# Performance work log

Measured on AMD Instinct MI355X. Metric: run time of the kernel, lower is better.

Reference implementation:

```python
import jax, jax.numpy as jnp
import numpy as np

BITS = 4
N_PACK = 32 // BITS  # int32 compression
GROUPSIZE = 128
MASK = (1 << BITS) - 1


def _unpack_int32(q, axis):
    """Unpack int32 tensor into N_PACK low-bit values along `axis`.
    Element j*N_PACK+e comes from bits [BITS*e, BITS*(e+1)) of packed word j."""
    parts = [ (q >> (BITS * e)) & MASK for e in range(N_PACK) ]
    u = jnp.stack(parts, axis=axis + 1)  # (..., P, N_PACK, ...)
    shape = list(q.shape)
    shape[axis] = shape[axis] * N_PACK
    return u.reshape(shape)


def setup_inputs() -> dict:
    key = jax.random.key(0)
    k1, k2, k3, k4, k5 = jax.random.split(key, 5)
    in_f, out_f = 4096, 12288
    tokens = 8192
    n_groups = in_f // GROUPSIZE  # 32
    x = jax.random.normal(k1, (tokens, in_f), dtype=jnp.float32)
    scales = jax.random.uniform(k2, (n_groups, out_f), dtype=jnp.float32) * 0.01 + 1e-3
    bias = jax.random.normal(k3, (out_f,), dtype=jnp.float32)
    qweight = jax.random.randint(k4, (in_f // N_PACK, out_f), jnp.iinfo(jnp.int32).min, jnp.iinfo(jnp.int32).max, dtype=jnp.int32)
    qzeros = jax.random.randint(k5, (n_groups, out_f // N_PACK), jnp.iinfo(jnp.int32).min, jnp.iinfo(jnp.int32).max, dtype=jnp.int32)
    return {"x": x, "scales": scales, "bias": bias, "qweight": qweight, "qzeros": qzeros}


def reference(x, scales, bias, qweight, qzeros):
    in_f = qweight.shape[0] * N_PACK
    out_f = qweight.shape[1]
    n_groups = scales.shape[0]
    # Unpack 4-bit weights along input-channel axis: (in_f, out_f), values 0..15
    w_int = _unpack_int32(qweight, axis=0).astype(scales.dtype)
    # Unpack zero points along output-channel axis; optimum format stores zp-1
    zp = (_unpack_int32(qzeros, axis=1) + 1).astype(scales.dtype)  # (n_groups, out_f)
    # Per-group dequant: group g covers input channels [g*GROUPSIZE, (g+1)*GROUPSIZE)
    w = (w_int.reshape(n_groups, GROUPSIZE, out_f) - zp[:, None, :]) * scales[:, None, :]
    w = w.reshape(in_f, out_f)
    # Linear: y = x @ W^T with W = w.T, i.e. x @ w
    return x @ w + bias
```

## Files before the change

kernel.cpp:

```cpp
#include <hip/hip_runtime.h>
#include <hip/hip_bf16.h>


typedef __attribute__((ext_vector_type(8))) short short8;
typedef __attribute__((ext_vector_type(4))) float f32x4;

__device__ __forceinline__ short f2bf(float f) {
  unsigned u = __float_as_uint(f);
  u += 0x7fffu + ((u >> 16) & 1u);
  return (short)(u >> 16);
}

__device__ __forceinline__ void gload_lds16(const void* g, void* l) {
  __builtin_amdgcn_global_load_lds(
      (const __attribute__((address_space(1))) void*)g,
      (__attribute__((address_space(3))) void*)l,
      16, 0, 0);
}

__device__ __forceinline__ void bar() {
  asm volatile("" ::: "memory");
  __builtin_amdgcn_s_barrier();
  asm volatile("" ::: "memory");
}
__device__ __forceinline__ void wait_vm3() {
  asm volatile("s_waitcnt vmcnt(3)" ::: "memory");
}
__device__ __forceinline__ void wait_vm0() {
  asm volatile("s_waitcnt vmcnt(0)" ::: "memory");
}

__global__ __launch_bounds__(256) void dequant_tile_kernel(
    const int* __restrict__ qweight, const int* __restrict__ qzeros,
    const float* __restrict__ scales, short* __restrict__ Bt,
    int N, int K) {
  const int ktn = K >> 5;
  const int bx = blockIdx.x;
  const int nb = bx / ktn, kt = bx - nb * ktn;
  const int t = threadIdx.x;
  const int g = kt >> 2;
  char* dst = (char*)Bt + (size_t)bx * 8192;
#pragma unroll
  for (int p = 0; p < 2; ++p) {
    const int c = p * 256 + t;
    const int l = c & 63;
    const int n = nb * 128 + (c >> 6) * 16 + (l & 15);
    const int kw = kt * 4 + (l >> 4);
    const float sc = scales[(size_t)g * N + n];
    const int zw = qzeros[(size_t)g * (N >> 3) + (n >> 3)];
    const float zs = -(float)(((zw >> ((n & 7) * 4)) & 15) + 1) * sc;
    const int w = qweight[(size_t)kw * N + n];
    short8 v;
#pragma unroll
    for (int e = 0; e < 8; ++e)
      v[e] = f2bf(fmaf((float)((w >> (4 * e)) & 15), sc, zs));
    *(short8*)(dst + c * 16) = v;
  }
}

__global__ __launch_bounds__(256) void cvt_tile_kernel(
    const float* __restrict__ x, short* __restrict__ xb, int K) {
  const int ktn = K >> 5;
  const int bx = blockIdx.x;
  const int mb = bx / ktn, kt = bx - mb * ktn;
  char* dst = (char*)xb + (size_t)bx * 16384;
#pragma unroll
  for (int p = 0; p < 4; ++p) {
    const int c = p * 256 + threadIdx.x;
    const int l = c & 63;
    const int row = mb * 256 + (c >> 6) * 16 + (l & 15);
    const int k = kt * 32 + (l >> 4) * 8;
    const float* s = x + (size_t)row * K + k;
    float4 f0 = *(const float4*)s;
    float4 f1 = *(const float4*)(s + 4);
    short8 v;
    v[0] = f2bf(f0.x); v[1] = f2bf(f0.y); v[2] = f2bf(f0.z); v[3] = f2bf(f0.w);
    v[4] = f2bf(f1.x); v[5] = f2bf(f1.y); v[6] = f2bf(f1.z); v[7] = f2bf(f1.w);
    *(short8*)(dst + c * 16) = v;
  }
}

#define GBM 256
#define GBN 128

__global__ __launch_bounds__(512, 4) void gemm256_kernel(
    const short* __restrict__ At, const short* __restrict__ Bt,
    const float* __restrict__ bias, float* __restrict__ C,
    int M, int N, int K) {
  __shared__ __align__(16) char lds[3 * 24576];
  const int tid = threadIdx.x;
  const int nbx = N / GBN;
  const int nwg = gridDim.x;
  int bid = blockIdx.x;
  if ((nwg & 7) == 0) bid = (bid & 7) * (nwg >> 3) + (bid >> 3);
  const int mb = bid / nbx;
  const int nb = bid % nbx;
  const int bm = mb * GBM, bn = nb * GBN;

  const int wid = tid >> 6, lane = tid & 63;
  const int wr = wid >> 2, wc = wid & 3;

  const int P = K >> 5;

  char* lb = &lds[0];

  const char* aBase = lb + wr * 8192 + lane * 16;
  const char* bBase = lb + 16384 + wc * 2048 + lane * 16;

  const char* pA = (const char*)At + (size_t)mb * P * 16384 + (size_t)tid * 16;
  const char* pB = (const char*)Bt + (size_t)nb * P * 8192 + (size_t)tid * 16;
  char* dA = lb + tid * 16;
  char* dB = lb + 16384 + tid * 16;

#define STAGE(TSL, AOFF, BOFF)                         \
  do {                                                 \
    gload_lds16(pA + (AOFF), dA + (TSL)*24576);        \
    gload_lds16(pA + (AOFF) + 8192, dA + (TSL)*24576 + 8192); \
    gload_lds16(pB + (BOFF), dB + (TSL)*24576);        \
  } while (0)

  short8 aR[8], bR[2];

#define RD(SL)                                                        \
  do {                                                                \
    _Pragma("unroll") for (int i = 0; i < 8; ++i) aR[i] =             \
        *(const short8*)(aBase + (SL)*24576 + i * 1024);              \
    _Pragma("unroll") for (int j = 0; j < 2; ++j) bR[j] =             \
        *(const short8*)(bBase + (SL)*24576 + j * 1024);              \
  } while (0)

  f32x4 acc[8][2] = {};

#define MFMA16()                                                      \
  do {                                                                \
    __builtin_amdgcn_s_setprio(1);                                    \
    _Pragma("unroll") for (int i = 0; i < 8; ++i)                     \
        _Pragma("unroll") for (int j = 0; j < 2; ++j) acc[i][j] =     \
            __builtin_amdgcn_mfma_f32_16x16x32_bf16(aR[i], bR[j],     \
                                                    acc[i][j], 0, 0, 0); \
    __builtin_amdgcn_s_setprio(0);                                    \
  } while (0)

  STAGE(0, 0, 0);
  STAGE(1, 16384, 8192);

  const int nIt = (P - 2) / 3;
  for (int it = 0; it < nIt; ++it) {
    wait_vm3(); bar();
    RD(0); STAGE(2, 2 * 16384, 2 * 8192); MFMA16();
    wait_vm3(); bar();
    RD(1); STAGE(0, 3 * 16384, 3 * 8192); MFMA16();
    wait_vm3(); bar();
    RD(2); STAGE(1, 4 * 16384, 4 * 8192); MFMA16();
    pA += 3 * 16384;
    pB += 3 * 8192;
  }
  wait_vm3(); bar();
  RD(0); MFMA16();
  wait_vm0(); bar();
  RD(1); MFMA16();

#undef MFMA16
#undef RD
#undef STAGE

  const int crow0 = bm + wr * 128 + (lane >> 4) * 4;
  const int ccol0 = bn + wc * 32 + (lane & 15);
#pragma unroll
  for (int fj = 0; fj < 2; ++fj) {
    const float bv = bias[ccol0 + fj * 16];
#pragma unroll
    for (int fi = 0; fi < 8; ++fi) {
#pragma unroll
      for (int r = 0; r < 4; ++r) {
        C[(size_t)(crow0 + fi * 16 + r) * N + ccol0 + fj * 16] =
            acc[fi][fj][r] + bv;
      }
    }
  }
}

__global__ __launch_bounds__(256) void dequant_kernel(
    const int* __restrict__ qweight, const int* __restrict__ qzeros,
    const float* __restrict__ scales, short* __restrict__ Wt,
    int in_f, int out_f) {
  __shared__ __align__(16) short T[64][72];
  const int n0 = blockIdx.x * 64;
  const int k0 = blockIdx.y * 64;
  const int t = threadIdx.x;
  const int nl = t & 63;
  const int kw = t >> 6;
  const int n = n0 + nl;
  const int g = k0 >> 7;
  const float sc = scales[(size_t)g * out_f + n];
  const int zpw = qzeros[(size_t)g * (out_f >> 3) + (n >> 3)];
  const float zp = (float)(((zpw >> ((n & 7) * 4)) & 15) + 1);
  const float zs = zp * sc;
#pragma unroll
  for (int rr = 0; rr < 2; ++rr) {
    const int kwi = kw + rr * 4;
    const int w = qweight[(size_t)((k0 >> 3) + kwi) * out_f + n];
    short8 v;
#pragma unroll
    for (int e = 0; e < 8; ++e) {
      float f = (float)((w >> (4 * e)) & 15) * sc - zs;
      v[e] = f2bf(f);
    }
    *(short8*)&T[nl][kwi * 8] = v;
  }
  __syncthreads();
#pragma unroll
  for (int rr = 0; rr < 2; ++rr) {
    const int c = rr * 256 + t;
    const int row = c >> 3, ch = c & 7;
    *(short8*)&Wt[(size_t)(n0 + row) * in_f + k0 + ch * 8] =
        *(const short8*)&T[row][ch * 8];
  }
}

__global__ __launch_bounds__(256) void cvt_kernel(
    const float* __restrict__ x, short* __restrict__ xb, long n8) {
  long i = (long)blockIdx.x * blockDim.x + threadIdx.x;
  if (i >= n8) return;
  const float* src = x + i * 8;
  float4 a = *(const float4*)src;
  float4 b = *(const float4*)(src + 4);
  short8 v;
  v[0] = f2bf(a.x); v[1] = f2bf(a.y); v[2] = f2bf(a.z); v[3] = f2bf(a.w);
  v[4] = f2bf(b.x); v[5] = f2bf(b.y); v[6] = f2bf(b.z); v[7] = f2bf(b.w);
  *(short8*)(xb + i * 8) = v;
}

#define BM 128
#define BN 128
#define BK 64

template <bool A_BF16>
__global__ __launch_bounds__(256) void gemm_bias_kernel(
    const void* __restrict__ Av, const short* __restrict__ Bt,
    const float* __restrict__ bias, float* __restrict__ C,
    int M, int N, int K) {
  __shared__ __align__(16) short As[BM * BK];
  __shared__ __align__(16) short Bs[BN * BK];
  const int tid = threadIdx.x;
  const int bm = blockIdx.y * BM;
  const int bn = blockIdx.x * BN;
  const int wid = tid >> 6, lane = tid & 63;
  const int wr = wid >> 1, wc = wid & 1;
  const int lrow = lane & 15;
  const int lk = (lane >> 4) * 8;

  f32x4 acc[4][4] = {};

  for (int kt = 0; kt < K; kt += BK) {
    if constexpr (A_BF16) {
      const short* A = (const short*)Av;
#pragma unroll
      for (int r = 0; r < 4; ++r) {
        const int c = r * 256 + tid;
        const int row = c >> 3, ch = c & 7;
        gload_lds16(A + (size_t)(bm + row) * K + kt + ch * 8,
                    (char*)As + c * 16);
      }
    } else {
      const float* A = (const float*)Av;
#pragma unroll
      for (int r = 0; r < 4; ++r) {
        const int c = r * 256 + tid;
        const int row = c >> 3, ch = c & 7;
        const float* src = A + (size_t)(bm + row) * K + kt + ch * 8;
        float4 f0 = *(const float4*)src;
        float4 f1 = *(const float4*)(src + 4);
        short8 v;
        v[0] = f2bf(f0.x); v[1] = f2bf(f0.y); v[2] = f2bf(f0.z); v[3] = f2bf(f0.w);
        v[4] = f2bf(f1.x); v[5] = f2bf(f1.y); v[6] = f2bf(f1.z); v[7] = f2bf(f1.w);
        *(short8*)((char*)As + c * 16) = v;
      }
    }
#pragma unroll
    for (int r = 0; r < 4; ++r) {
      const int c = r * 256 + tid;
      const int row = c >> 3, ch = c & 7;
      gload_lds16(Bt + (size_t)(bn + row) * K + kt + ch * 8,
                  (char*)Bs + c * 16);
    }
    __syncthreads();
#pragma unroll
    for (int kk = 0; kk < 2; ++kk) {
      short8 af[4], bf[4];
#pragma unroll
      for (int i = 0; i < 4; ++i)
        af[i] = *(const short8*)&As[(wr * 64 + i * 16 + lrow) * BK + kk * 32 + lk];
#pragma unroll
      for (int j = 0; j < 4; ++j)
        bf[j] = *(const short8*)&Bs[(wc * 64 + j * 16 + lrow) * BK + kk * 32 + lk];
#pragma unroll
      for (int i = 0; i < 4; ++i)
#pragma unroll
        for (int j = 0; j < 4; ++j)
          acc[i][j] = __builtin_amdgcn_mfma_f32_16x16x32_bf16(
              af[i], bf[j], acc[i][j], 0, 0, 0);
    }
    __syncthreads();
  }

  const int crow0 = bm + wr * 64 + (lane >> 4) * 4;
  const int ccol0 = bn + wc * 64 + (lane & 15);
#pragma unroll
  for (int j = 0; j < 4; ++j) {
    const float bv = bias[ccol0 + j * 16];
#pragma unroll
    for (int i = 0; i < 4; ++i) {
#pragma unroll
      for (int r = 0; r < 4; ++r) {
        C[(size_t)(crow0 + i * 16 + r) * N + ccol0 + j * 16] = acc[i][j][r] + bv;
      }
    }
  }
}

__global__ __launch_bounds__(256) void naive_kernel(
    const float* __restrict__ x, const float* __restrict__ scales,
    const float* __restrict__ bias, const int* __restrict__ qw,
    const int* __restrict__ qz, float* __restrict__ out,
    int M, int K, int N) {
  long idx = (long)blockIdx.x * blockDim.x + threadIdx.x;
  if (idx >= (long)M * N) return;
  const int n = (int)(idx % N);
  const int m = (int)(idx / N);
  float acc = 0.f;
  for (int g = 0; g < K / 128; ++g) {
    const float sc = scales[(size_t)g * N + n];
    const float zp =
        (float)(((qz[(size_t)g * (N >> 3) + (n >> 3)] >> ((n & 7) * 4)) & 15) + 1);
    const float zs = zp * sc;
    for (int kw = 0; kw < 16; ++kw) {
      const int w = qw[(size_t)(g * 16 + kw) * N + n];
      const float* xp = &x[(size_t)m * K + g * 128 + kw * 8];
#pragma unroll
      for (int e = 0; e < 8; ++e)
        acc += xp[e] * ((float)((w >> (4 * e)) & 15) * sc - zs);
    }
  }
  out[idx] = acc + bias[n];
}

extern "C" void kernel_launch(void* const* d_in, const int* in_sizes, int n_in,
                              void* d_out, int out_size, void* d_ws,
                              size_t ws_size, hipStream_t stream) {
  const float* x = (const float*)d_in[0];
  const float* scales = (const float*)d_in[1];
  const float* bias = (const float*)d_in[2];
  const int* qweight = (const int*)d_in[3];
  const int* qzeros = (const int*)d_in[4];
  float* out = (float*)d_out;

  const int out_f = in_sizes[2];
  const int kwords = in_sizes[3] / out_f;
  const int in_f = kwords * 8;
  const int tokens = in_sizes[0] / in_f;
  const int M = tokens, K = in_f, N = out_f;

  const size_t wt_bytes = (size_t)K * N * sizeof(short);
  const size_t xb_bytes = (size_t)M * K * sizeof(short);

  const bool div128 = (M % BM == 0) && (N % BN == 0) && (K % BK == 0) &&
                      (K % 128 == 0) && (N % 64 == 0);
  const bool divR16 = (M % GBM == 0) && (N % GBN == 0) && (K % 256 == 0) &&
                      (((K >> 5) - 2) % 3 == 0);

  if (divR16 && ws_size >= wt_bytes + xb_bytes) {
    short* Btile = (short*)d_ws;
    short* Atile = (short*)((char*)d_ws + wt_bytes);
    const int ktn = K >> 5;
    dequant_tile_kernel<<<(N / 128) * ktn, 256, 0, stream>>>(
        qweight, qzeros, scales, Btile, N, K);
    cvt_tile_kernel<<<(M / 256) * ktn, 256, 0, stream>>>(x, Atile, K);
    gemm256_kernel<<<(M / GBM) * (N / GBN), 512, 0, stream>>>(
        Atile, Btile, bias, out, M, N, K);
  } else if (div128 && ws_size >= wt_bytes + xb_bytes) {
    short* Wt = (short*)d_ws;
    short* xb = (short*)((char*)d_ws + wt_bytes);
    dequant_kernel<<<dim3(N / 64, K / 64), 256, 0, stream>>>(
        qweight, qzeros, scales, Wt, K, N);
    const long n8 = (long)M * K / 8;
    cvt_kernel<<<(int)((n8 + 255) / 256), 256, 0, stream>>>(x, xb, n8);
    gemm_bias_kernel<true><<<dim3(N / BN, M / BM), 256, 0, stream>>>(
        xb, Wt, bias, out, M, N, K);
  } else if (div128 && ws_size >= wt_bytes) {
    short* Wt = (short*)d_ws;
    dequant_kernel<<<dim3(N / 64, K / 64), 256, 0, stream>>>(
        qweight, qzeros, scales, Wt, K, N);
    gemm_bias_kernel<false><<<dim3(N / BN, M / BM), 256, 0, stream>>>(
        x, Wt, bias, out, M, N, K);
  } else {
    const long total = (long)M * N;
    naive_kernel<<<(int)((total + 255) / 256), 256, 0, stream>>>(
        x, scales, bias, qweight, qzeros, out, M, K, N);
  }
}
```

Baseline: 771.2 us.

## Switch GEMM to 32x32x16 bf16 MFMA with matching pre-tiled operand layouts

Replaces the 16x16x32 MFMA tiling in the main GEMM with 32x32x16 MFMAs: each wave now holds four 32x32 accumulators instead of sixteen 16x16 ones. The dequant and conversion tile kernels reorder their output so the pre-tiled A and B layouts match the new operand fragment mapping. The epilogue store indexing changes to the 32x32 accumulator layout. The aim is fewer MFMA instructions and LDS reads per tile and higher matrix-core throughput. The risk is a changed register and LDS access pattern and a layout mismatch that would give wrong results.

```diff
diff --git a/kernel.cpp b/kernel.cpp
--- a/kernel.cpp
+++ b/kernel.cpp
@@ -4,6 +4,7 @@
 
 typedef __attribute__((ext_vector_type(8))) short short8;
 typedef __attribute__((ext_vector_type(4))) float f32x4;
+typedef __attribute__((ext_vector_type(16))) float f32x16;
 
 __device__ __forceinline__ short f2bf(float f) {
   unsigned u = __float_as_uint(f);
@@ -43,9 +44,9 @@
 #pragma unroll
   for (int p = 0; p < 2; ++p) {
     const int c = p * 256 + t;
-    const int l = c & 63;
-    const int n = nb * 128 + (c >> 6) * 16 + (l & 15);
-    const int kw = kt * 4 + (l >> 4);
+    const int n = nb * 128 + (c >> 7) * 32 + (c & 31);
+    const int k8 = ((c >> 6) & 1) * 2 + ((c >> 5) & 1);
+    const int kw = kt * 4 + k8;
     const float sc = scales[(size_t)g * N + n];
     const int zw = qzeros[(size_t)g * (N >> 3) + (n >> 3)];
     const float zs = -(float)(((zw >> ((n & 7) * 4)) & 15) + 1) * sc;
@@ -67,9 +68,8 @@
 #pragma unroll
   for (int p = 0; p < 4; ++p) {
     const int c = p * 256 + threadIdx.x;
-    const int l = c & 63;
-    const int row = mb * 256 + (c >> 6) * 16 + (l & 15);
-    const int k = kt * 32 + (l >> 4) * 8;
+    const int row = mb * 256 + (c >> 7) * 32 + (c & 31);
+    const int k = kt * 32 + ((c >> 6) & 1) * 16 + ((c >> 5) & 1) * 8;
     const float* s = x + (size_t)row * K + k;
     float4 f0 = *(const float4*)s;
     float4 f1 = *(const float4*)(s + 4);
@@ -99,6 +99,8 @@
 
   const int wid = tid >> 6, lane = tid & 63;
   const int wr = wid >> 2, wc = wid & 3;
+  const int l31 = lane & 31;
+  const int lq2 = lane >> 5;
 
   const int P = K >> 5;
 
@@ -112,33 +114,34 @@
   char* dA = lb + tid * 16;
   char* dB = lb + 16384 + tid * 16;
 
-#define STAGE(TSL, AOFF, BOFF)                         \
-  do {                                                 \
-    gload_lds16(pA + (AOFF), dA + (TSL)*24576);        \
+#define STAGE(TSL, AOFF, BOFF)                                \
+  do {                                                        \
+    gload_lds16(pA + (AOFF), dA + (TSL)*24576);               \
     gload_lds16(pA + (AOFF) + 8192, dA + (TSL)*24576 + 8192); \
-    gload_lds16(pB + (BOFF), dB + (TSL)*24576);        \
+    gload_lds16(pB + (BOFF), dB + (TSL)*24576);               \
   } while (0)
 
-  short8 aR[8], bR[2];
-
-#define RD(SL)                                                        \
-  do {                                                                \
-    _Pragma("unroll") for (int i = 0; i < 8; ++i) aR[i] =             \
-        *(const short8*)(aBase + (SL)*24576 + i * 1024);              \
-    _Pragma("unroll") for (int j = 0; j < 2; ++j) bR[j] =             \
-        *(const short8*)(bBase + (SL)*24576 + j * 1024);              \
+  short8 aR[4][2], bR[2];
+
+#define RD(SL)                                                            \
+  do {                                                                    \
+    _Pragma("unroll") for (int i = 0; i < 4; ++i)                         \
+        _Pragma("unroll") for (int kh = 0; kh < 2; ++kh) aR[i][kh] =      \
+        *(const short8*)(aBase + (SL)*24576 + i * 2048 + kh * 1024);      \
+    _Pragma("unroll") for (int kh = 0; kh < 2; ++kh) bR[kh] =             \
+        *(const short8*)(bBase + (SL)*24576 + kh * 1024);                 \
   } while (0)
 
-  f32x4 acc[8][2] = {};
-
-#define MFMA16()                                                      \
-  do {                                                                \
-    __builtin_amdgcn_s_setprio(1);                                    \
-    _Pragma("unroll") for (int i = 0; i < 8; ++i)                     \
-        _Pragma("unroll") for (int j = 0; j < 2; ++j) acc[i][j] =     \
-            __builtin_amdgcn_mfma_f32_16x16x32_bf16(aR[i], bR[j],     \
-                                                    acc[i][j], 0, 0, 0); \
-    __builtin_amdgcn_s_setprio(0);                                    \
+  f32x16 acc[4] = {};
+
+#define MFMA8()                                                           \
+  do {                                                                    \
+    __builtin_amdgcn_s_setprio(1);                                        \
+    _Pragma("unroll") for (int kh = 0; kh < 2; ++kh)                      \
+        _Pragma("unroll") for (int i = 0; i < 4; ++i) acc[i] =            \
+            __builtin_amdgcn_mfma_f32_32x32x16_bf16(aR[i][kh], bR[kh],    \
+                                                    acc[i], 0, 0, 0);     \
+    __builtin_amdgcn_s_setprio(0);                                        \
   } while (0)
 
   STAGE(0, 0, 0);
@@ -147,35 +150,32 @@
   const int nIt = (P - 2) / 3;
   for (int it = 0; it < nIt; ++it) {
     wait_vm3(); bar();
-    RD(0); STAGE(2, 2 * 16384, 2 * 8192); MFMA16();
+    RD(0); STAGE(2, 2 * 16384, 2 * 8192); MFMA8();
     wait_vm3(); bar();
-    RD(1); STAGE(0, 3 * 16384, 3 * 8192); MFMA16();
+    RD(1); STAGE(0, 3 * 16384, 3 * 8192); MFMA8();
     wait_vm3(); bar();
-    RD(2); STAGE(1, 4 * 16384, 4 * 8192); MFMA16();
+    RD(2); STAGE(1, 4 * 16384, 4 * 8192); MFMA8();
     pA += 3 * 16384;
     pB += 3 * 8192;
   }
   wait_vm3(); bar();
-  RD(0); MFMA16();
+  RD(0); MFMA8();
   wait_vm0(); bar();
-  RD(1); MFMA16();
-
-#undef MFMA16
+  RD(1); MFMA8();
+
+#undef MFMA8
 #undef RD
 #undef STAGE
 
-  const int crow0 = bm + wr * 128 + (lane >> 4) * 4;
-  const int ccol0 = bn + wc * 32 + (lane & 15);
-#pragma unroll
-  for (int fj = 0; fj < 2; ++fj) {
-    const float bv = bias[ccol0 + fj * 16];
-#pragma unroll
-    for (int fi = 0; fi < 8; ++fi) {
-#pragma unroll
-      for (int r = 0; r < 4; ++r) {
-        C[(size_t)(crow0 + fi * 16 + r) * N + ccol0 + fj * 16] =
-            acc[fi][fj][r] + bv;
-      }
+  const int crow0 = bm + wr * 128 + 4 * lq2;
+  const int ccol = bn + wc * 32 + l31;
+  const float bv = bias[ccol];
+#pragma unroll
+  for (int i = 0; i < 4; ++i) {
+#pragma unroll
+    for (int reg = 0; reg < 16; ++reg) {
+      const int row = crow0 + i * 32 + (reg & 3) + 8 * (reg >> 2);
+      C[(size_t)row * N + ccol] = acc[i][reg] + bv;
     }
   }
 }
@@ -366,10 +366,10 @@
 
   const bool div128 = (M % BM == 0) && (N % BN == 0) && (K % BK == 0) &&
                       (K % 128 == 0) && (N % 64 == 0);
-  const bool divR16 = (M % GBM == 0) && (N % GBN == 0) && (K % 256 == 0) &&
+  const bool divR17 = (M % GBM == 0) && (N % GBN == 0) && (K % 256 == 0) &&
                       (((K >> 5) - 2) % 3 == 0);
 
-  if (divR16 && ws_size >= wt_bytes + xb_bytes) {
+  if (divR17 && ws_size >= wt_bytes + xb_bytes) {
     short* Btile = (short*)d_ws;
     short* Atile = (short*)((char*)d_ws + wt_bytes);
     const int ktn = K >> 5;
```

Measured after the change: 905.3 us. 1.17x slower.
